# Optimization experiments

Measured on AMD Instinct MI355X. Metric: run time of the kernel, lower is better.

## Reference

```python
import math
import jax, jax.numpy as jnp
import numpy as np

B, S, D, L = 8, 4096, 1024, 16

def setup_inputs() -> dict:
    key = jax.random.key(0)
    k1, k2, k3 = jax.random.split(key, 3)
    memory = jax.random.normal(k1, (B, S, D), dtype=jnp.float32)
    summarizer = jax.random.normal(k2, (L, D), dtype=jnp.float32) * 0.02
    w_proj = jax.random.normal(k3, (1, L), dtype=jnp.float32) * (1.0 / math.sqrt(L))
    return {"memory": memory, "summarizer": summarizer, "w_proj": w_proj}

def reference(memory, summarizer, w_proj):
    # scores: [B, L, S] = summarizer @ memory^T / sqrt(D)
    d = summarizer.shape[-1]
    scores = jnp.einsum('ld,bsd->bls', summarizer, memory) / jnp.sqrt(jnp.asarray(d, memory.dtype))
    p_attn = jax.nn.softmax(scores, axis=-1)            # softmax over sequence S
    ctx = jnp.einsum('bls,bsd->bld', p_attn, memory)    # [B, L, D]
    # nn.Linear(L, 1, bias=False) applied to ctx.transpose(-1,-2): [B, D, L] @ W^T -> [B, D, 1]
    out = jnp.einsum('bld,l->bd', ctx, w_proj[0])       # [B, D]
    return out[:, None, :]                              # [B, 1, D] after final transpose
```

## Files before the change

### kernel.cpp

```cpp
#include <hip/hip_runtime.h>
#include <hip/hip_bf16.h>

#define BB 8
#define SS 4096
#define DD 1024
#define LL 16

typedef __attribute__((ext_vector_type(8))) short short8;
typedef __attribute__((ext_vector_type(4))) float fl4;

static __device__ __forceinline__ short f2bf(float f) {
    unsigned u = __float_as_uint(f);
    u += 0x7FFFu + ((u >> 16) & 1u);
    return (short)(u >> 16);
}

__global__ __launch_bounds__(256) void k_prep(const float* __restrict__ summ,
                                              short* __restrict__ summb,
                                              float* __restrict__ Z,
                                              float* __restrict__ out) {
    int i = blockIdx.x * 256 + threadIdx.x;
    if (i < LL * DD) summb[i] = f2bf(summ[i]);
    if (i < BB * LL) Z[i] = 0.f;
    if (i < BB * DD) out[i] = 0.f;
}

__global__ __launch_bounds__(256) void k_scores(const float* __restrict__ mem,
                                                const short* __restrict__ summb,
                                                float* __restrict__ e,
                                                float* __restrict__ Z) {
    int widx  = threadIdx.x >> 6;
    int gwave = blockIdx.x * 4 + widx;
    int lane  = threadIdx.x & 63;
    int b     = gwave >> 8;
    int s0    = (gwave & 255) << 4;
    int o  = lane & 15;
    int qd = lane >> 4;

    const short* arow = summb + o * DD + qd * 8;
    const float* mrow = mem + ((size_t)b * SS + (size_t)(s0 + o)) * DD + qd * 8;

    fl4 acc = {0.f, 0.f, 0.f, 0.f};
    #pragma unroll 8
    for (int k = 0; k < DD; k += 32) {
        short8 a = *(const short8*)(arow + k);
        fl4 f0 = *(const fl4*)(mrow + k);
        fl4 f1 = *(const fl4*)(mrow + k + 4);
        short8 bb;
        bb[0] = f2bf(f0[0]); bb[1] = f2bf(f0[1]);
        bb[2] = f2bf(f0[2]); bb[3] = f2bf(f0[3]);
        bb[4] = f2bf(f1[0]); bb[5] = f2bf(f1[1]);
        bb[6] = f2bf(f1[2]); bb[7] = f2bf(f1[3]);
        acc = __builtin_amdgcn_mfma_f32_16x16x32_bf16(a, bb, acc, 0, 0, 0);
    }

    const float scale = 0.03125f;
    float ev[4];
    float* ebase = e + ((size_t)b * SS + s0) * LL;
    #pragma unroll
    for (int r = 0; r < 4; ++r) {
        ev[r] = __expf(acc[r] * scale);
        ebase[o * LL + qd * 4 + r] = ev[r];
    }

    #pragma unroll
    for (int r = 0; r < 4; ++r) {
        float v = ev[r];
        v += __shfl_xor(v, 1, 64);
        v += __shfl_xor(v, 2, 64);
        v += __shfl_xor(v, 4, 64);
        v += __shfl_xor(v, 8, 64);
        ev[r] = v;
    }
    __shared__ float zp[4][LL];
    if (o == 0) {
        #pragma unroll
        for (int r = 0; r < 4; ++r) zp[widx][qd * 4 + r] = ev[r];
    }
    __syncthreads();
    int t = threadIdx.x;
    if (t < LL) {
        float v = zp[0][t] + zp[1][t] + zp[2][t] + zp[3][t];
        atomicAdd(&Z[b * LL + t], v);
    }
}

__global__ __launch_bounds__(256) void k_ctx(const float* __restrict__ mem,
                                             const float* __restrict__ e,
                                             const float* __restrict__ Z,
                                             const float* __restrict__ w,
                                             float* __restrict__ out) {
    int blk = blockIdx.x;
    int b  = blk >> 6;
    int ch = blk & 63;
    int t = threadIdx.x;
    int s0 = ch * 64;

    __shared__ float coef[LL];
    __shared__ float qs[64];
    if (t < LL) coef[t] = w[t] / Z[b * LL + t];
    __syncthreads();
    if (t < 64) {
        const float* ep = e + ((size_t)b * SS + s0 + t) * LL;
        float qv = 0.f;
        #pragma unroll
        for (int l = 0; l < LL; ++l) qv += coef[l] * ep[l];
        qs[t] = qv;
    }
    __syncthreads();

    const float* mb = mem + ((size_t)b * SS + s0) * DD + t * 4;
    fl4 acc = {0.f, 0.f, 0.f, 0.f};
    #pragma unroll 8
    for (int i = 0; i < 64; ++i) {
        fl4 m4 = *(const fl4*)(mb + (size_t)i * DD);
        acc += qs[i] * m4;
    }
    float* op = out + (size_t)b * DD + t * 4;
    atomicAdd(op + 0, acc[0]);
    atomicAdd(op + 1, acc[1]);
    atomicAdd(op + 2, acc[2]);
    atomicAdd(op + 3, acc[3]);
}

extern "C" void kernel_launch(void* const* d_in, const int* in_sizes, int n_in,
                              void* d_out, int out_size, void* d_ws, size_t ws_size,
                              hipStream_t stream) {
    const float* mem  = (const float*)d_in[0];
    const float* summ = (const float*)d_in[1];
    const float* w    = (const float*)d_in[2];
    float* out = (float*)d_out;

    char* ws = (char*)d_ws;
    short* summb = (short*)ws;
    float* Z     = (float*)(ws + 64 * 1024);
    float* e     = (float*)(ws + 68 * 1024);

    k_prep<<<64, 256, 0, stream>>>(summ, summb, Z, out);
    k_scores<<<(BB * SS / 16) / 4, 256, 0, stream>>>(mem, summb, e, Z);
    k_ctx<<<BB * 64, 256, 0, stream>>>(mem, e, Z, w, out);
}
```

Measured before the change: 219.7 us.

## Fuse score and context passes so each block reuses its memory chunk

Merges the score computation and the context accumulation into one kernel per 64-row chunk. The unnormalised exp weights stay in LDS, and the block computes per-chunk partial contexts for all 16 summarizer rows, with Z normalisation deferred to a second reduction kernel. This replaces the global e buffer, the atomics and the separate prep kernel. The aim is for the second read of memory to hit cache right after the first, instead of streaming the 128MB input twice. The cost is a 32MB partial-context buffer written and then read back, plus each block converting the summarizer to bf16 in LDS.

```diff
diff --git a/kernel.cpp b/kernel.cpp
--- a/kernel.cpp
+++ b/kernel.cpp
@@ -5,6 +5,7 @@
 #define SS 4096
 #define DD 1024
 #define LL 16
+#define SPAD 1032
 
 typedef __attribute__((ext_vector_type(8))) short short8;
 typedef __attribute__((ext_vector_type(4))) float fl4;
@@ -15,30 +16,35 @@
     return (short)(u >> 16);
 }
 
-__global__ __launch_bounds__(256) void k_prep(const float* __restrict__ summ,
-                                              short* __restrict__ summb,
-                                              float* __restrict__ Z,
-                                              float* __restrict__ out) {
-    int i = blockIdx.x * 256 + threadIdx.x;
-    if (i < LL * DD) summb[i] = f2bf(summ[i]);
-    if (i < BB * LL) Z[i] = 0.f;
-    if (i < BB * DD) out[i] = 0.f;
-}
+__global__ __launch_bounds__(256) void k_fused(const float* __restrict__ mem,
+                                               const float* __restrict__ summ,
+                                               float* __restrict__ part,
+                                               float* __restrict__ Zpart) {
+    __shared__ short summ_l[LL * SPAD];
+    __shared__ float e_lds[64 * LL];
+    __shared__ float zp[4][LL];
 
-__global__ __launch_bounds__(256) void k_scores(const float* __restrict__ mem,
-                                                const short* __restrict__ summb,
-                                                float* __restrict__ e,
-                                                float* __restrict__ Z) {
-    int widx  = threadIdx.x >> 6;
-    int gwave = blockIdx.x * 4 + widx;
-    int lane  = threadIdx.x & 63;
-    int b     = gwave >> 8;
-    int s0    = (gwave & 255) << 4;
+    int blk = blockIdx.x;
+    int b   = blk >> 6;
+    int s0  = (blk & 63) << 6;
+    int t    = threadIdx.x;
+    int w    = t >> 6;
+    int lane = t & 63;
     int o  = lane & 15;
     int qd = lane >> 4;
 
-    const short* arow = summb + o * DD + qd * 8;
-    const float* mrow = mem + ((size_t)b * SS + (size_t)(s0 + o)) * DD + qd * 8;
+    for (int i = t; i < LL * DD / 4; i += 256) {
+        int l = i >> 8, d = (i & 255) * 4;
+        fl4 v = *(const fl4*)(summ + l * DD + d);
+        short tmp[4];
+        tmp[0] = f2bf(v[0]); tmp[1] = f2bf(v[1]);
+        tmp[2] = f2bf(v[2]); tmp[3] = f2bf(v[3]);
+        *(unsigned long long*)&summ_l[l * SPAD + d] = *(unsigned long long*)tmp;
+    }
+    __syncthreads();
+
+    const short* arow = summ_l + o * SPAD + qd * 8;
+    const float* mrow = mem + ((size_t)b * SS + s0 + w * 16 + o) * DD + qd * 8;
 
     fl4 acc = {0.f, 0.f, 0.f, 0.f};
     #pragma unroll 8
@@ -55,72 +61,86 @@
     }
 
     const float scale = 0.03125f;
-    float ev[4];
-    float* ebase = e + ((size_t)b * SS + s0) * LL;
+    fl4 ev;
+    #pragma unroll
+    for (int r = 0; r < 4; ++r) ev[r] = __expf(acc[r] * scale);
+    *(fl4*)&e_lds[(w * 16 + o) * LL + qd * 4] = ev;
+
+    fl4 zs = ev;
     #pragma unroll
     for (int r = 0; r < 4; ++r) {
-        ev[r] = __expf(acc[r] * scale);
-        ebase[o * LL + qd * 4 + r] = ev[r];
-    }
-
-    #pragma unroll
-    for (int r = 0; r < 4; ++r) {
-        float v = ev[r];
+        float v = zs[r];
         v += __shfl_xor(v, 1, 64);
         v += __shfl_xor(v, 2, 64);
         v += __shfl_xor(v, 4, 64);
         v += __shfl_xor(v, 8, 64);
-        ev[r] = v;
+        zs[r] = v;
     }
-    __shared__ float zp[4][LL];
-    if (o == 0) {
+    if (o == 0) *(fl4*)&zp[w][qd * 4] = zs;
+    __syncthreads();
+
+    fl4 ctx[LL];
+    #pragma unroll
+    for (int l = 0; l < LL; ++l) ctx[l] = (fl4){0.f, 0.f, 0.f, 0.f};
+    const float* mb = mem + ((size_t)b * SS + s0) * DD + t * 4;
+    #pragma unroll 4
+    for (int s = 0; s < 64; ++s) {
+        fl4 m4 = *(const fl4*)(mb + (size_t)s * DD);
+        const fl4* ee = (const fl4*)&e_lds[s * LL];
         #pragma unroll
-        for (int r = 0; r < 4; ++r) zp[widx][qd * 4 + r] = ev[r];
+        for (int g = 0; g < 4; ++g) {
+            fl4 e4 = ee[g];
+            ctx[g * 4 + 0] += e4[0] * m4;
+            ctx[g * 4 + 1] += e4[1] * m4;
+            ctx[g * 4 + 2] += e4[2] * m4;
+            ctx[g * 4 + 3] += e4[3] * m4;
+        }
     }
-    __syncthreads();
-    int t = threadIdx.x;
-    if (t < LL) {
-        float v = zp[0][t] + zp[1][t] + zp[2][t] + zp[3][t];
-        atomicAdd(&Z[b * LL + t], v);
-    }
+    float* pp = part + (size_t)blk * LL * DD + t * 4;
+    #pragma unroll
+    for (int l = 0; l < LL; ++l) *(fl4*)(pp + l * DD) = ctx[l];
+    if (t < LL) Zpart[blk * LL + t] = zp[0][t] + zp[1][t] + zp[2][t] + zp[3][t];
 }
 
-__global__ __launch_bounds__(256) void k_ctx(const float* __restrict__ mem,
-                                             const float* __restrict__ e,
-                                             const float* __restrict__ Z,
+__global__ __launch_bounds__(256) void k_out(const float* __restrict__ part,
+                                             const float* __restrict__ Zpart,
                                              const float* __restrict__ w,
                                              float* __restrict__ out) {
-    int blk = blockIdx.x;
-    int b  = blk >> 6;
-    int ch = blk & 63;
+    int blkid = blockIdx.x;
+    int b  = blkid >> 4;
+    int d0 = (blkid & 15) << 6;
     int t = threadIdx.x;
-    int s0 = ch * 64;
+    __shared__ float zz[16][LL];
+    __shared__ float coef[LL];
+    __shared__ float red[4][64];
 
-    __shared__ float coef[LL];
-    __shared__ float qs[64];
-    if (t < LL) coef[t] = w[t] / Z[b * LL + t];
+    int l = t & 15, cq = t >> 4;
+    float zsum = 0.f;
+    #pragma unroll
+    for (int j = 0; j < 4; ++j) zsum += Zpart[(b * 64 + cq * 4 + j) * LL + l];
+    zz[cq][l] = zsum;
     __syncthreads();
-    if (t < 64) {
-        const float* ep = e + ((size_t)b * SS + s0 + t) * LL;
-        float qv = 0.f;
+    if (t < LL) {
+        float Z = 0.f;
         #pragma unroll
-        for (int l = 0; l < LL; ++l) qv += coef[l] * ep[l];
-        qs[t] = qv;
+        for (int g = 0; g < 16; ++g) Z += zz[g][t];
+        coef[t] = w[t] / Z;
     }
     __syncthreads();
 
-    const float* mb = mem + ((size_t)b * SS + s0) * DD + t * 4;
-    fl4 acc = {0.f, 0.f, 0.f, 0.f};
-    #pragma unroll 8
-    for (int i = 0; i < 64; ++i) {
-        fl4 m4 = *(const fl4*)(mb + (size_t)i * DD);
-        acc += qs[i] * m4;
+    float c[LL];
+    #pragma unroll
+    for (int i = 0; i < LL; ++i) c[i] = coef[i];
+    int doff = t & 63, cg = t >> 6;
+    float accv = 0.f;
+    for (int ch = cg * 16; ch < cg * 16 + 16; ++ch) {
+        const float* pb = part + (size_t)(b * 64 + ch) * LL * DD + d0 + doff;
+        #pragma unroll
+        for (int l2 = 0; l2 < LL; ++l2) accv += c[l2] * pb[(size_t)l2 * DD];
     }
-    float* op = out + (size_t)b * DD + t * 4;
-    atomicAdd(op + 0, acc[0]);
-    atomicAdd(op + 1, acc[1]);
-    atomicAdd(op + 2, acc[2]);
-    atomicAdd(op + 3, acc[3]);
+    red[cg][doff] = accv;
+    __syncthreads();
+    if (t < 64) out[b * DD + d0 + t] = red[0][t] + red[1][t] + red[2][t] + red[3][t];
 }
 
 extern "C" void kernel_launch(void* const* d_in, const int* in_sizes, int n_in,
@@ -132,11 +152,9 @@
     float* out = (float*)d_out;
 
     char* ws = (char*)d_ws;
-    short* summb = (short*)ws;
-    float* Z     = (float*)(ws + 64 * 1024);
-    float* e     = (float*)(ws + 68 * 1024);
+    float* Zpart = (float*)ws;
+    float* part  = (float*)(ws + 64 * 1024);
 
-    k_prep<<<64, 256, 0, stream>>>(summ, summb, Z, out);
-    k_scores<<<(BB * SS / 16) / 4, 256, 0, stream>>>(mem, summb, e, Z);
-    k_ctx<<<BB * 64, 256, 0, stream>>>(mem, e, Z, w, out);
+    k_fused<<<BB * 64, 256, 0, stream>>>(mem, summ, part, Zpart);
+    k_out<<<BB * 16, 256, 0, stream>>>(part, Zpart, w, out);
 }
```

New measurement: 237.3 us. +8.0%, slower.

## Split-K score waves with LDS reduction and prefetch loads in both passes

Applied to the files above, without the earlier changes.

The scores kernel now gives each 16-row tile to two waves, each covering half of D. The halves are combined through shared memory, and the next fp32 memory chunk is loaded before the current one is converted. The context kernel uses 32-row chunks over twice as many blocks, with a one-ahead prefetch, and the barrier between the coef and qs computations is gone. The aim is more waves in flight and more latency hiding on a bandwidth-bound pass, at the cost of an extra block barrier and LDS round trip in the scores kernel and twice as many output atomics.

```diff
diff --git a/kernel.cpp b/kernel.cpp
--- a/kernel.cpp
+++ b/kernel.cpp
@@ -25,82 +25,88 @@
     if (i < BB * DD) out[i] = 0.f;
 }
 
-__global__ __launch_bounds__(256) void k_scores(const float* __restrict__ mem,
-                                                const short* __restrict__ summb,
-                                                float* __restrict__ e,
-                                                float* __restrict__ Z) {
-    int widx  = threadIdx.x >> 6;
-    int gwave = blockIdx.x * 4 + widx;
-    int lane  = threadIdx.x & 63;
-    int b     = gwave >> 8;
-    int s0    = (gwave & 255) << 4;
+__global__ __launch_bounds__(256, 4) void k_scores(const float* __restrict__ mem,
+                                                   const short* __restrict__ summb,
+                                                   float* __restrict__ e,
+                                                   float* __restrict__ Z) {
+    __shared__ float red[2][64 * 4];
+    int widx = threadIdx.x >> 6;
+    int tp   = widx >> 1;
+    int h    = widx & 1;
+    int tile = blockIdx.x * 2 + tp;
+    int lane = threadIdx.x & 63;
+    int b  = tile >> 8;
+    int s0 = (tile & 255) << 4;
     int o  = lane & 15;
     int qd = lane >> 4;
+    int kb = h << 9;
 
-    const short* arow = summb + o * DD + qd * 8;
-    const float* mrow = mem + ((size_t)b * SS + (size_t)(s0 + o)) * DD + qd * 8;
+    const short* arow = summb + o * DD + kb + qd * 8;
+    const float* mrow = mem + ((size_t)b * SS + s0 + o) * DD + kb + qd * 8;
 
     fl4 acc = {0.f, 0.f, 0.f, 0.f};
-    #pragma unroll 8
-    for (int k = 0; k < DD; k += 32) {
-        short8 a = *(const short8*)(arow + k);
-        fl4 f0 = *(const fl4*)(mrow + k);
-        fl4 f1 = *(const fl4*)(mrow + k + 4);
+    fl4 p0 = *(const fl4*)(mrow);
+    fl4 p1 = *(const fl4*)(mrow + 4);
+    #pragma unroll
+    for (int i = 0; i < 16; ++i) {
+        fl4 n0, n1;
+        if (i < 15) {
+            n0 = *(const fl4*)(mrow + (i + 1) * 32);
+            n1 = *(const fl4*)(mrow + (i + 1) * 32 + 4);
+        }
+        short8 a = *(const short8*)(arow + i * 32);
         short8 bb;
-        bb[0] = f2bf(f0[0]); bb[1] = f2bf(f0[1]);
-        bb[2] = f2bf(f0[2]); bb[3] = f2bf(f0[3]);
-        bb[4] = f2bf(f1[0]); bb[5] = f2bf(f1[1]);
-        bb[6] = f2bf(f1[2]); bb[7] = f2bf(f1[3]);
+        bb[0] = f2bf(p0[0]); bb[1] = f2bf(p0[1]);
+        bb[2] = f2bf(p0[2]); bb[3] = f2bf(p0[3]);
+        bb[4] = f2bf(p1[0]); bb[5] = f2bf(p1[1]);
+        bb[6] = f2bf(p1[2]); bb[7] = f2bf(p1[3]);
         acc = __builtin_amdgcn_mfma_f32_16x16x32_bf16(a, bb, acc, 0, 0, 0);
+        p0 = n0; p1 = n1;
     }
 
-    const float scale = 0.03125f;
-    float ev[4];
-    float* ebase = e + ((size_t)b * SS + s0) * LL;
-    #pragma unroll
-    for (int r = 0; r < 4; ++r) {
-        ev[r] = __expf(acc[r] * scale);
-        ebase[o * LL + qd * 4 + r] = ev[r];
-    }
+    if (h == 1) *(fl4*)&red[tp][lane * 4] = acc;
+    __syncthreads();
+    if (h == 0) {
+        fl4 other = *(const fl4*)&red[tp][lane * 4];
+        acc += other;
 
-    #pragma unroll
-    for (int r = 0; r < 4; ++r) {
-        float v = ev[r];
-        v += __shfl_xor(v, 1, 64);
-        v += __shfl_xor(v, 2, 64);
-        v += __shfl_xor(v, 4, 64);
-        v += __shfl_xor(v, 8, 64);
-        ev[r] = v;
-    }
-    __shared__ float zp[4][LL];
-    if (o == 0) {
+        const float scale = 0.03125f;
+        fl4 ev;
         #pragma unroll
-        for (int r = 0; r < 4; ++r) zp[widx][qd * 4 + r] = ev[r];
-    }
-    __syncthreads();
-    int t = threadIdx.x;
-    if (t < LL) {
-        float v = zp[0][t] + zp[1][t] + zp[2][t] + zp[3][t];
-        atomicAdd(&Z[b * LL + t], v);
+        for (int r = 0; r < 4; ++r) ev[r] = __expf(acc[r] * scale);
+        *(fl4*)&e[((size_t)b * SS + s0 + o) * LL + qd * 4] = ev;
+
+        fl4 zs = ev;
+        #pragma unroll
+        for (int r = 0; r < 4; ++r) {
+            float v = zs[r];
+            v += __shfl_xor(v, 1, 64);
+            v += __shfl_xor(v, 2, 64);
+            v += __shfl_xor(v, 4, 64);
+            v += __shfl_xor(v, 8, 64);
+            zs[r] = v;
+        }
+        if (o == 0) {
+            #pragma unroll
+            for (int r = 0; r < 4; ++r) atomicAdd(&Z[b * LL + qd * 4 + r], zs[r]);
+        }
     }
 }
 
-__global__ __launch_bounds__(256) void k_ctx(const float* __restrict__ mem,
-                                             const float* __restrict__ e,
-                                             const float* __restrict__ Z,
-                                             const float* __restrict__ w,
-                                             float* __restrict__ out) {
+__global__ __launch_bounds__(256, 4) void k_ctx(const float* __restrict__ mem,
+                                                const float* __restrict__ e,
+                                                const float* __restrict__ Z,
+                                                const float* __restrict__ w,
+                                                float* __restrict__ out) {
     int blk = blockIdx.x;
-    int b  = blk >> 6;
-    int ch = blk & 63;
+    int b  = blk >> 7;
+    int s0 = (blk & 127) << 5;
     int t = threadIdx.x;
-    int s0 = ch * 64;
 
     __shared__ float coef[LL];
-    __shared__ float qs[64];
+    __shared__ float qs[32];
     if (t < LL) coef[t] = w[t] / Z[b * LL + t];
-    __syncthreads();
-    if (t < 64) {
+    if (t < 32) {
         const float* ep = e + ((size_t)b * SS + s0 + t) * LL;
         float qv = 0.f;
         #pragma unroll
@@ -111,10 +117,13 @@
 
     const float* mb = mem + ((size_t)b * SS + s0) * DD + t * 4;
     fl4 acc = {0.f, 0.f, 0.f, 0.f};
-    #pragma unroll 8
-    for (int i = 0; i < 64; ++i) {
-        fl4 m4 = *(const fl4*)(mb + (size_t)i * DD);
-        acc += qs[i] * m4;
+    fl4 c = *(const fl4*)(mb);
+    #pragma unroll
+    for (int i = 0; i < 32; ++i) {
+        fl4 n;
+        if (i < 31) n = *(const fl4*)(mb + (size_t)(i + 1) * DD);
+        acc += qs[i] * c;
+        c = n;
     }
     float* op = out + (size_t)b * DD + t * 4;
     atomicAdd(op + 0, acc[0]);
@@ -137,6 +146,6 @@
     float* e     = (float*)(ws + 68 * 1024);
 
     k_prep<<<64, 256, 0, stream>>>(summ, summb, Z, out);
-    k_scores<<<(BB * SS / 16) / 4, 256, 0, stream>>>(mem, summb, e, Z);
-    k_ctx<<<BB * 64, 256, 0, stream>>>(mem, e, Z, w, out);
+    k_scores<<<1024, 256, 0, stream>>>(mem, summb, e, Z);
+    k_ctx<<<1024, 256, 0, stream>>>(mem, e, Z, w, out);
 }
```

Result: slower. 254.6 us (+15.9%).
